# Performance work log

Measured on AMD Instinct MI355X. Metric: run time of the kernel, lower is better.

## Reference

```python
import jax, jax.numpy as jnp
import numpy as np
import math

B, L, D, N = 8, 4096, 1024, 16

def setup_inputs() -> dict:
    key = jax.random.key(0)
    k1, k2, k3, k4, k5, k6 = jax.random.split(key, 6)
    return {
        "x": jax.random.normal(k1, (B, L, D), dtype=jnp.float32),
        "delta": jax.random.normal(k2, (D, N, 1), dtype=jnp.float32),
        "alpha": jax.random.normal(k3, (D, N, 1), dtype=jnp.float32),
        "beta": jax.random.normal(k4, (D, N, 1), dtype=jnp.float32),
        "gamma": jax.random.normal(k5, (D, N), dtype=jnp.float32),
        "omega": jax.random.normal(k6, (D,), dtype=jnp.float32),
    }

def reference(x, delta, alpha, beta, gamma, omega):
    # x: (B, L, D). Unidirectional EMA, no state, no padding mask.
    b, l, d = x.shape
    n_state = gamma.shape[-1]
    scale = math.sqrt(1.0 / n_state)

    residual = x * omega  # (B, L, D)
    xt = jnp.swapaxes(x, -1, -2)  # (B, D, L)

    # EMA coefficients
    p = jax.nn.sigmoid(delta)          # (D, N, 1)
    a = jax.nn.sigmoid(alpha)          # (D, N, 1)
    q = 1.0 - p * a                    # (D, N, 1)

    # Vandermonde kernel: k[d, t] = sum_n p*beta*q^t * gamma*scale
    t = jnp.arange(l, dtype=x.dtype)   # (L,)
    vander = t[None, None, :] * jnp.log(q)          # (D, N, L)
    kernel = p * beta * jnp.exp(vander)             # (D, N, L)
    k = jnp.einsum('dnl,dn->dl', kernel, gamma * scale)  # (D, L)

    # FFT long convolution with zero-padding to 2L (linear conv)
    n_fft = 2 * l
    k_f = jnp.fft.rfft(k, n=n_fft)                  # (D, L+1) complex
    x_f = jnp.fft.rfft(xt, n=n_fft)                 # (B, D, L+1) complex
    out = jnp.fft.irfft(x_f * k_f, n=n_fft)[..., :l]  # (B, D, L)

    return jnp.swapaxes(out, -1, -2) + residual     # (B, L, D)
```

## Files before the change

kernel.cpp:

```cpp
#include <hip/hip_runtime.h>

#define BB 8
#define LL 4096
#define DD 1024
#define NN 16
#define UF 8

__device__ __forceinline__ float sigmoid_precise(float v) {
    return 1.0f / (1.0f + expf(-v));
}

template <int G_>
__global__ __launch_bounds__(256) void ema_chunk_states(
    const float* __restrict__ x,
    const float* __restrict__ delta,
    const float* __restrict__ alpha,
    float* __restrict__ E)
{
    constexpr int C_ = LL / G_;
    const int g = blockIdx.x;
    const int d = blockIdx.y * 256 + threadIdx.x;
    const int b = blockIdx.z;

    float q[NN];
#pragma unroll
    for (int n = 0; n < NN; ++n) {
        float p = sigmoid_precise(delta[d * NN + n]);
        float a = sigmoid_precise(alpha[d * NN + n]);
        q[n] = 1.0f - p * a;
    }

    float u[NN];
#pragma unroll
    for (int n = 0; n < NN; ++n) u[n] = 0.0f;

    const float* xp = x + ((size_t)b * LL + (size_t)g * C_) * DD + d;
    for (int ii = 0; ii < C_; ii += UF) {
        float xv[UF];
#pragma unroll
        for (int j = 0; j < UF; ++j)
            xv[j] = xp[(size_t)(ii + j) * DD];
#pragma unroll
        for (int j = 0; j < UF; ++j) {
#pragma unroll
            for (int n = 0; n < NN; ++n)
                u[n] = fmaf(q[n], u[n], xv[j]);
        }
    }

    float* Ep = E + (((size_t)b * G_ + g) * NN) * DD + d;
#pragma unroll
    for (int n = 0; n < NN; ++n)
        Ep[(size_t)n * DD] = u[n];
}

template <int G_>
__global__ __launch_bounds__(256) void ema_carry_scan(
    const float* __restrict__ delta,
    const float* __restrict__ alpha,
    float* __restrict__ E)
{
    constexpr int C_ = LL / G_;
    const int t = blockIdx.x * 256 + threadIdx.x;
    const int d = t & (DD - 1);
    const int n = (t >> 10) & (NN - 1);
    const int b = t >> 14;

    const float p = sigmoid_precise(delta[d * NN + n]);
    const float a = sigmoid_precise(alpha[d * NN + n]);
    const float q = 1.0f - p * a;
    const float Qc = powf(q, (float)C_);

    float* Ep = E + (((size_t)b * G_) * NN + n) * DD + d;
    const size_t gstride = (size_t)NN * DD;

    float u = 0.0f;
    for (int gg = 0; gg < G_; gg += UF) {
        float ev[UF], sv[UF];
#pragma unroll
        for (int j = 0; j < UF; ++j)
            ev[j] = Ep[(size_t)(gg + j) * gstride];
#pragma unroll
        for (int j = 0; j < UF; ++j) {
            u = fmaf(Qc, u, ev[j]);
            sv[j] = u;
        }
#pragma unroll
        for (int j = 0; j < UF; ++j)
            Ep[(size_t)(gg + j) * gstride] = sv[j];
    }
}

template <int G_>
__global__ __launch_bounds__(256) void ema_final(
    const float* __restrict__ x,
    const float* __restrict__ delta,
    const float* __restrict__ alpha,
    const float* __restrict__ beta,
    const float* __restrict__ gamma,
    const float* __restrict__ omega,
    const float* __restrict__ S,
    float* __restrict__ out)
{
    constexpr int C_ = LL / G_;
    const int g = blockIdx.x;
    const int d = blockIdx.y * 256 + threadIdx.x;
    const int b = blockIdx.z;

    float q[NN], gc[NN];
#pragma unroll
    for (int n = 0; n < NN; ++n) {
        float p = sigmoid_precise(delta[d * NN + n]);
        float a = sigmoid_precise(alpha[d * NN + n]);
        q[n]  = 1.0f - p * a;
        gc[n] = p * beta[d * NN + n] * gamma[d * NN + n] * 0.25f;
    }

    float u[NN];
    if (g > 0) {
        const float* Sp = S + (((size_t)b * G_ + (g - 1)) * NN) * DD + d;
#pragma unroll
        for (int n = 0; n < NN; ++n)
            u[n] = Sp[(size_t)n * DD];
    } else {
#pragma unroll
        for (int n = 0; n < NN; ++n) u[n] = 0.0f;
    }

    const float om = omega[d];
    const float* xp = x + ((size_t)b * LL + (size_t)g * C_) * DD + d;
    float* op = out + ((size_t)b * LL + (size_t)g * C_) * DD + d;

    for (int ii = 0; ii < C_; ii += UF) {
        float xv[UF];
#pragma unroll
        for (int j = 0; j < UF; ++j)
            xv[j] = xp[(size_t)(ii + j) * DD];
#pragma unroll
        for (int j = 0; j < UF; ++j) {
            float xvj = xv[j];
            float a0 = om * xvj, a1 = 0.0f, a2 = 0.0f, a3 = 0.0f;
#pragma unroll
            for (int n = 0; n < NN; n += 4) {
                u[n + 0] = fmaf(q[n + 0], u[n + 0], xvj);
                u[n + 1] = fmaf(q[n + 1], u[n + 1], xvj);
                u[n + 2] = fmaf(q[n + 2], u[n + 2], xvj);
                u[n + 3] = fmaf(q[n + 3], u[n + 3], xvj);
                a0 = fmaf(gc[n + 0], u[n + 0], a0);
                a1 = fmaf(gc[n + 1], u[n + 1], a1);
                a2 = fmaf(gc[n + 2], u[n + 2], a2);
                a3 = fmaf(gc[n + 3], u[n + 3], a3);
            }
            op[(size_t)(ii + j) * DD] = (a0 + a1) + (a2 + a3);
        }
    }
}

template <int G_>
static void launch_all(const float* x, const float* delta, const float* alpha,
                       const float* beta, const float* gamma, const float* omega,
                       float* out, float* E, hipStream_t stream)
{
    dim3 block(256);
    dim3 grid13(G_, DD / 256, BB);
    dim3 grid2((BB * NN * DD) / 256);
    hipLaunchKernelGGL(ema_chunk_states<G_>, grid13, block, 0, stream,
                       x, delta, alpha, E);
    hipLaunchKernelGGL(ema_carry_scan<G_>, grid2, block, 0, stream,
                       delta, alpha, E);
    hipLaunchKernelGGL(ema_final<G_>, grid13, block, 0, stream,
                       x, delta, alpha, beta, gamma, omega, E, out);
}

extern "C" void kernel_launch(void* const* d_in, const int* in_sizes, int n_in,
                              void* d_out, int out_size, void* d_ws, size_t ws_size,
                              hipStream_t stream) {
    const float* x     = (const float*)d_in[0];
    const float* delta = (const float*)d_in[1];
    const float* alpha = (const float*)d_in[2];
    const float* beta  = (const float*)d_in[3];
    const float* gamma = (const float*)d_in[4];
    const float* omega = (const float*)d_in[5];
    float* out = (float*)d_out;
    float* E = (float*)d_ws;

    const size_t need64 = (size_t)BB * 64 * NN * DD * sizeof(float);
    if (ws_size >= need64)
        launch_all<64>(x, delta, alpha, beta, gamma, omega, out, E, stream);
    else
        launch_all<32>(x, delta, alpha, beta, gamma, omega, out, E, stream);
}
```

Baseline: 297.8 us.

## Fuse three-stage chunked EMA scan into one persistent kernel with grid barriers

Replaces the three kernel launches (chunk states, carry scan, final output) with a single persistent kernel of 512 blocks. The phases are separated by atomic-counter grid barriers, and intermediate states move through system-coherent loads and stores. Each block handles several chunks, and the carry power is computed by repeated squaring instead of powf. The aim is to remove launch gaps and inter-kernel drain. In exchange it relies on all 512 blocks being co-resident (2 per CU requested), adds a memset, and bypasses caches on state traffic.

```diff
diff --git a/kernel.cpp b/kernel.cpp
--- a/kernel.cpp
+++ b/kernel.cpp
@@ -1,175 +1,216 @@
 #include <hip/hip_runtime.h>
+
 
 #define BB 8
 #define LL 4096
 #define DD 1024
 #define NN 16
 #define UF 8
+#define NB 512
 
 __device__ __forceinline__ float sigmoid_precise(float v) {
     return 1.0f / (1.0f + expf(-v));
 }
 
+__device__ __forceinline__ void sc_store(float* p, float v) {
+    asm volatile("global_store_dword %0, %1, off sc0 sc1"
+                 :: "v"(p), "v"(v) : "memory");
+}
+__device__ __forceinline__ int sc_load_i(const int* p) {
+    int v;
+    asm volatile("global_load_dword %0, %1, off sc0 sc1\n\t"
+                 "s_waitcnt vmcnt(0)"
+                 : "=v"(v) : "v"(p) : "memory");
+    return v;
+}
+__device__ __forceinline__ void sc_load4(const float* p0, const float* p1,
+                                         const float* p2, const float* p3,
+                                         float& o0, float& o1, float& o2, float& o3) {
+    asm volatile(
+        "global_load_dword %0, %4, off sc0 sc1\n\t"
+        "global_load_dword %1, %5, off sc0 sc1\n\t"
+        "global_load_dword %2, %6, off sc0 sc1\n\t"
+        "global_load_dword %3, %7, off sc0 sc1\n\t"
+        "s_waitcnt vmcnt(0)"
+        : "=&v"(o0), "=&v"(o1), "=&v"(o2), "=&v"(o3)
+        : "v"(p0), "v"(p1), "v"(p2), "v"(p3)
+        : "memory");
+}
+__device__ __forceinline__ void sc_load8s(const float* p, size_t stride, float* o) {
+    const float* a0 = p;
+    const float* a1 = p + stride;
+    const float* a2 = p + 2 * stride;
+    const float* a3 = p + 3 * stride;
+    const float* a4 = p + 4 * stride;
+    const float* a5 = p + 5 * stride;
+    const float* a6 = p + 6 * stride;
+    const float* a7 = p + 7 * stride;
+    asm volatile(
+        "global_load_dword %0, %8, off sc0 sc1\n\t"
+        "global_load_dword %1, %9, off sc0 sc1\n\t"
+        "global_load_dword %2, %10, off sc0 sc1\n\t"
+        "global_load_dword %3, %11, off sc0 sc1\n\t"
+        "global_load_dword %4, %12, off sc0 sc1\n\t"
+        "global_load_dword %5, %13, off sc0 sc1\n\t"
+        "global_load_dword %6, %14, off sc0 sc1\n\t"
+        "global_load_dword %7, %15, off sc0 sc1\n\t"
+        "s_waitcnt vmcnt(0)"
+        : "=&v"(o[0]), "=&v"(o[1]), "=&v"(o[2]), "=&v"(o[3]),
+          "=&v"(o[4]), "=&v"(o[5]), "=&v"(o[6]), "=&v"(o[7])
+        : "v"(a0), "v"(a1), "v"(a2), "v"(a3),
+          "v"(a4), "v"(a5), "v"(a6), "v"(a7)
+        : "memory");
+}
+__device__ __forceinline__ void vm_drain() {
+    asm volatile("s_waitcnt vmcnt(0)" ::: "memory");
+}
+
+__device__ __forceinline__ void grid_barrier(int* bar) {
+    vm_drain();
+    __syncthreads();
+    if (threadIdx.x == 0) {
+        atomicAdd(bar, 1);
+        while (sc_load_i(bar) < NB)
+            __builtin_amdgcn_s_sleep(2);
+    }
+    __syncthreads();
+}
+
 template <int G_>
-__global__ __launch_bounds__(256) void ema_chunk_states(
-    const float* __restrict__ x,
-    const float* __restrict__ delta,
-    const float* __restrict__ alpha,
-    float* __restrict__ E)
-{
-    constexpr int C_ = LL / G_;
-    const int g = blockIdx.x;
-    const int d = blockIdx.y * 256 + threadIdx.x;
-    const int b = blockIdx.z;
-
-    float q[NN];
-#pragma unroll
-    for (int n = 0; n < NN; ++n) {
-        float p = sigmoid_precise(delta[d * NN + n]);
-        float a = sigmoid_precise(alpha[d * NN + n]);
-        q[n] = 1.0f - p * a;
-    }
-
-    float u[NN];
-#pragma unroll
-    for (int n = 0; n < NN; ++n) u[n] = 0.0f;
-
-    const float* xp = x + ((size_t)b * LL + (size_t)g * C_) * DD + d;
-    for (int ii = 0; ii < C_; ii += UF) {
-        float xv[UF];
-#pragma unroll
-        for (int j = 0; j < UF; ++j)
-            xv[j] = xp[(size_t)(ii + j) * DD];
-#pragma unroll
-        for (int j = 0; j < UF; ++j) {
-#pragma unroll
-            for (int n = 0; n < NN; ++n)
-                u[n] = fmaf(q[n], u[n], xv[j]);
-        }
-    }
-
-    float* Ep = E + (((size_t)b * G_ + g) * NN) * DD + d;
-#pragma unroll
-    for (int n = 0; n < NN; ++n)
-        Ep[(size_t)n * DD] = u[n];
-}
-
-template <int G_>
-__global__ __launch_bounds__(256) void ema_carry_scan(
-    const float* __restrict__ delta,
-    const float* __restrict__ alpha,
-    float* __restrict__ E)
-{
-    constexpr int C_ = LL / G_;
-    const int t = blockIdx.x * 256 + threadIdx.x;
-    const int d = t & (DD - 1);
-    const int n = (t >> 10) & (NN - 1);
-    const int b = t >> 14;
-
-    const float p = sigmoid_precise(delta[d * NN + n]);
-    const float a = sigmoid_precise(alpha[d * NN + n]);
-    const float q = 1.0f - p * a;
-    const float Qc = powf(q, (float)C_);
-
-    float* Ep = E + (((size_t)b * G_) * NN + n) * DD + d;
-    const size_t gstride = (size_t)NN * DD;
-
-    float u = 0.0f;
-    for (int gg = 0; gg < G_; gg += UF) {
-        float ev[UF], sv[UF];
-#pragma unroll
-        for (int j = 0; j < UF; ++j)
-            ev[j] = Ep[(size_t)(gg + j) * gstride];
-#pragma unroll
-        for (int j = 0; j < UF; ++j) {
-            u = fmaf(Qc, u, ev[j]);
-            sv[j] = u;
-        }
-#pragma unroll
-        for (int j = 0; j < UF; ++j)
-            Ep[(size_t)(gg + j) * gstride] = sv[j];
-    }
-}
-
-template <int G_>
-__global__ __launch_bounds__(256) void ema_final(
+__global__ __launch_bounds__(256, 2) void ema_onepass(
     const float* __restrict__ x,
     const float* __restrict__ delta,
     const float* __restrict__ alpha,
     const float* __restrict__ beta,
     const float* __restrict__ gamma,
     const float* __restrict__ omega,
-    const float* __restrict__ S,
-    float* __restrict__ out)
+    float* __restrict__ out,
+    float* __restrict__ E,
+    int*   __restrict__ bar)
 {
-    constexpr int C_ = LL / G_;
-    const int g = blockIdx.x;
-    const int d = blockIdx.y * 256 + threadIdx.x;
-    const int b = blockIdx.z;
+    constexpr int C_    = LL / G_;
+    constexpr int NTASK = (32 * G_) / NB;
+    static_assert((C_ & (C_ - 1)) == 0, "C_ must be a power of two");
+    static_assert(32 * G_ == NB * NTASK, "task tiling must be exact");
+
+    const int blk   = blockIdx.x;
+    const int chain = blk & 31;
+    const int b     = chain >> 2;
+    const int dblk  = chain & 3;
+    const int d     = dblk * 256 + threadIdx.x;
 
     float q[NN], gc[NN];
 #pragma unroll
     for (int n = 0; n < NN; ++n) {
-        float p = sigmoid_precise(delta[d * NN + n]);
-        float a = sigmoid_precise(alpha[d * NN + n]);
+        const float p = sigmoid_precise(delta[d * NN + n]);
+        const float a = sigmoid_precise(alpha[d * NN + n]);
         q[n]  = 1.0f - p * a;
         gc[n] = p * beta[d * NN + n] * gamma[d * NN + n] * 0.25f;
     }
-
-    float u[NN];
-    if (g > 0) {
-        const float* Sp = S + (((size_t)b * G_ + (g - 1)) * NN) * DD + d;
+    const float om = omega[d];
+
+    for (int k = 0; k < NTASK; ++k) {
+        const int g = (blk >> 5) + k * (G_ / NTASK);
+        const float* xp = x + ((size_t)b * LL + (size_t)g * C_) * DD + d;
+
+        float u[NN];
+#pragma unroll
+        for (int n = 0; n < NN; ++n) u[n] = 0.0f;
+        for (int ii = 0; ii < C_; ii += UF) {
+            float xv[UF];
+#pragma unroll
+            for (int j = 0; j < UF; ++j)
+                xv[j] = xp[(size_t)(ii + j) * DD];
+#pragma unroll
+            for (int j = 0; j < UF; ++j)
+#pragma unroll
+                for (int n = 0; n < NN; ++n)
+                    u[n] = fmaf(q[n], u[n], xv[j]);
+        }
+        float* Ep = E + (((size_t)b * G_ + g) * NN) * DD + d;
 #pragma unroll
         for (int n = 0; n < NN; ++n)
-            u[n] = Sp[(size_t)n * DD];
-    } else {
-#pragma unroll
-        for (int n = 0; n < NN; ++n) u[n] = 0.0f;
-    }
-
-    const float om = omega[d];
-    const float* xp = x + ((size_t)b * LL + (size_t)g * C_) * DD + d;
-    float* op = out + ((size_t)b * LL + (size_t)g * C_) * DD + d;
-
-    for (int ii = 0; ii < C_; ii += UF) {
-        float xv[UF];
-#pragma unroll
-        for (int j = 0; j < UF; ++j)
-            xv[j] = xp[(size_t)(ii + j) * DD];
-#pragma unroll
-        for (int j = 0; j < UF; ++j) {
-            float xvj = xv[j];
-            float a0 = om * xvj, a1 = 0.0f, a2 = 0.0f, a3 = 0.0f;
-#pragma unroll
-            for (int n = 0; n < NN; n += 4) {
-                u[n + 0] = fmaf(q[n + 0], u[n + 0], xvj);
-                u[n + 1] = fmaf(q[n + 1], u[n + 1], xvj);
-                u[n + 2] = fmaf(q[n + 2], u[n + 2], xvj);
-                u[n + 3] = fmaf(q[n + 3], u[n + 3], xvj);
-                a0 = fmaf(gc[n + 0], u[n + 0], a0);
-                a1 = fmaf(gc[n + 1], u[n + 1], a1);
-                a2 = fmaf(gc[n + 2], u[n + 2], a2);
-                a3 = fmaf(gc[n + 3], u[n + 3], a3);
+            sc_store(Ep + (size_t)n * DD, u[n]);
+    }
+
+    grid_barrier(&bar[0]);
+
+    {
+        const int tt = blk * 256 + threadIdx.x;
+        const int sd = tt & (DD - 1);
+        const int sn = (tt >> 10) & (NN - 1);
+        const int sb = tt >> 14;
+
+        const float sp = sigmoid_precise(delta[sd * NN + sn]);
+        const float sa = sigmoid_precise(alpha[sd * NN + sn]);
+        const float sq = 1.0f - sp * sa;
+        float Qc = sq;
+#pragma unroll
+        for (int s2 = 1; s2 < C_; s2 <<= 1) Qc *= Qc;
+
+        float* Ep = E + ((size_t)sb * G_ * NN + sn) * DD + sd;
+        const size_t gs = (size_t)NN * DD;
+
+        float u = 0.0f;
+        for (int gg = 0; gg < G_; gg += UF) {
+            float ev[UF];
+            sc_load8s(Ep + (size_t)gg * gs, gs, ev);
+            float sv[UF];
+#pragma unroll
+            for (int j = 0; j < UF; ++j) {
+                u = fmaf(Qc, u, ev[j]);
+                sv[j] = u;
             }
-            op[(size_t)(ii + j) * DD] = (a0 + a1) + (a2 + a3);
-        }
-    }
-}
-
-template <int G_>
-static void launch_all(const float* x, const float* delta, const float* alpha,
-                       const float* beta, const float* gamma, const float* omega,
-                       float* out, float* E, hipStream_t stream)
-{
-    dim3 block(256);
-    dim3 grid13(G_, DD / 256, BB);
-    dim3 grid2((BB * NN * DD) / 256);
-    hipLaunchKernelGGL(ema_chunk_states<G_>, grid13, block, 0, stream,
-                       x, delta, alpha, E);
-    hipLaunchKernelGGL(ema_carry_scan<G_>, grid2, block, 0, stream,
-                       delta, alpha, E);
-    hipLaunchKernelGGL(ema_final<G_>, grid13, block, 0, stream,
-                       x, delta, alpha, beta, gamma, omega, E, out);
+#pragma unroll
+            for (int j = 0; j < UF; ++j)
+                sc_store(Ep + (size_t)(gg + j) * gs, sv[j]);
+        }
+    }
+
+    grid_barrier(&bar[1]);
+
+    for (int k = 0; k < NTASK; ++k) {
+        const int g = (blk >> 5) + k * (G_ / NTASK);
+        const float* xp = x + ((size_t)b * LL + (size_t)g * C_) * DD + d;
+        float*       op = out + ((size_t)b * LL + (size_t)g * C_) * DD + d;
+
+        float u[NN];
+        if (g > 0) {
+            const float* Sp = E + (((size_t)b * G_ + (g - 1)) * NN) * DD + d;
+#pragma unroll
+            for (int n = 0; n < NN; n += 4)
+                sc_load4(Sp + (size_t)(n + 0) * DD, Sp + (size_t)(n + 1) * DD,
+                         Sp + (size_t)(n + 2) * DD, Sp + (size_t)(n + 3) * DD,
+                         u[n + 0], u[n + 1], u[n + 2], u[n + 3]);
+        } else {
+#pragma unroll
+            for (int n = 0; n < NN; ++n) u[n] = 0.0f;
+        }
+
+        for (int ii = 0; ii < C_; ii += UF) {
+            float xv[UF];
+#pragma unroll
+            for (int j = 0; j < UF; ++j)
+                xv[j] = xp[(size_t)(ii + j) * DD];
+#pragma unroll
+            for (int j = 0; j < UF; ++j) {
+                const float xvj = xv[j];
+                float a0 = om * xvj, a1 = 0.0f, a2 = 0.0f, a3 = 0.0f;
+#pragma unroll
+                for (int n = 0; n < NN; n += 4) {
+                    u[n + 0] = fmaf(q[n + 0], u[n + 0], xvj);
+                    u[n + 1] = fmaf(q[n + 1], u[n + 1], xvj);
+                    u[n + 2] = fmaf(q[n + 2], u[n + 2], xvj);
+                    u[n + 3] = fmaf(q[n + 3], u[n + 3], xvj);
+                    a0 = fmaf(gc[n + 0], u[n + 0], a0);
+                    a1 = fmaf(gc[n + 1], u[n + 1], a1);
+                    a2 = fmaf(gc[n + 2], u[n + 2], a2);
+                    a3 = fmaf(gc[n + 3], u[n + 3], a3);
+                }
+                op[(size_t)(ii + j) * DD] = (a0 + a1) + (a2 + a3);
+            }
+        }
+    }
 }
 
 extern "C" void kernel_launch(void* const* d_in, const int* in_sizes, int n_in,
@@ -182,11 +223,17 @@
     const float* gamma = (const float*)d_in[4];
     const float* omega = (const float*)d_in[5];
     float* out = (float*)d_out;
-    float* E = (float*)d_ws;
-
-    const size_t need64 = (size_t)BB * 64 * NN * DD * sizeof(float);
+
+    int*   bar = (int*)d_ws;
+    float* E   = (float*)((char*)d_ws + 256);
+
+    hipMemsetAsync(d_ws, 0, 256, stream);
+
+    const size_t need64 = 256 + (size_t)BB * 64 * NN * DD * sizeof(float);
     if (ws_size >= need64)
-        launch_all<64>(x, delta, alpha, beta, gamma, omega, out, E, stream);
+        hipLaunchKernelGGL(ema_onepass<64>, dim3(NB), dim3(256), 0, stream,
+                           x, delta, alpha, beta, gamma, omega, out, E, bar);
     else
-        launch_all<32>(x, delta, alpha, beta, gamma, omega, out, E, stream);
-}
+        hipLaunchKernelGGL(ema_onepass<32>, dim3(NB), dim3(256), 0, stream,
+                           x, delta, alpha, beta, gamma, omega, out, E, bar);
+}
```

Measured after the change: 341.3 us. 1.15x slower.
